# Kernel tuning notes

Hardware: AMD Instinct MI355X
Metric: run time of the kernel (lower is better)

The kernel has to match this reference:

```python
import jax, jax.numpy as jnp
import numpy as np

N = 50000; FIN = 64; H = 128; E = 800000; T = 8
P = 250000; D = 500000; G = 20000; V = 2000; O = 2


def _mp(h, Ws, Wn, b, edge_src, edge_dst, n):
    # mean-aggregation message passing: relu(h Ws + mean_neigh(h) Wn + b)
    deg = jax.ops.segment_sum(jnp.ones(edge_dst.shape[0], h.dtype), edge_dst, n)
    agg = jax.ops.segment_sum(h[edge_src], edge_dst, n) / jnp.maximum(deg, 1.0)[:, None]
    return jax.nn.relu(h @ Ws + agg @ Wn + b)


def _forward(x, W_enc_self, W_enc_nei, b_enc, W2_self, W2_nei, b2, Wd1, bd1, Wd2, bd2,
             counts, edge_src, edge_dst, place_idx, src_idx, t_idx, dst_nodes, dst_seg,
             group_id, variant_of_group):
    n = x.shape[0]
    p = place_idx.shape[0]
    g = variant_of_group.shape[0]
    v = counts.shape[0]
    # first encoder, then T sequential second_encoder applications (feature generations)
    h0 = _mp(x, W_enc_self, W_enc_nei, b_enc, edge_src, edge_dst, n)

    def step(h, _):
        h2 = _mp(h, W2_self, W2_nei, b2, edge_src, edge_dst, n)
        return h2, h2

    _, hs = jax.lax.scan(step, h0, None, length=T)
    feats = jnp.concatenate([h0[None], hs], axis=0)  # [T+1, N, H]

    # gather (place, src) features at the generation index of each prediction
    place_f = feats[t_idx, place_idx]                 # [P, H]
    src_f = feats[t_idx, src_idx]                     # [P, H]
    # dst feature = sum over the destination set of each prediction
    dst_f = jax.ops.segment_sum(feats[t_idx[dst_seg], dst_nodes], dst_seg, p)  # [P, H]

    cat = jnp.concatenate([place_f, src_f, dst_f], axis=-1)  # [P, 3H]
    logits = jax.nn.relu(cat @ Wd1 + bd1) @ Wd2 + bd2        # [P, O]
    logprob = jax.nn.log_softmax(logits, axis=-1)            # [P, O]

    # prev_prob: inclusive running sum of per-step logprob sums within each variant
    group_sums = jax.ops.segment_sum(logprob, group_id, g)   # [G, O]
    cum = jnp.cumsum(group_sums, axis=0)
    var_tot = jax.ops.segment_sum(group_sums, variant_of_group, v)
    var_excl = jnp.cumsum(var_tot, axis=0) - var_tot
    within = cum - var_excl[variant_of_group]                # [G, O]
    prev = within[group_id]                                  # [P, O]

    logc = jnp.log(counts / jnp.sum(counts))                 # log(count/total) per variant
    add = logprob + prev + logc[variant_of_group[group_id]][:, None]
    return jnp.zeros((n, logits.shape[-1]), x.dtype).at[place_idx].add(add)


def setup_inputs() -> dict:
    ks = jax.random.split(jax.random.key(0), 24)
    s = jnp.float32(0.05)
    f32 = jnp.float32
    i32 = jnp.int32
    return {
        "x": jax.random.normal(ks[0], (N, FIN), f32),
        "W_enc_self": jax.random.normal(ks[1], (FIN, H), f32) * s,
        "W_enc_nei": jax.random.normal(ks[2], (FIN, H), f32) * s,
        "b_enc": jax.random.normal(ks[3], (H,), f32) * s,
        "W2_self": jax.random.normal(ks[4], (H, H), f32) * s,
        "W2_nei": jax.random.normal(ks[5], (H, H), f32) * s,
        "b2": jax.random.normal(ks[6], (H,), f32) * s,
        "Wd1": jax.random.normal(ks[7], (3 * H, 3 * H), f32) * s,
        "bd1": jax.random.normal(ks[8], (3 * H,), f32) * s,
        "Wd2": jax.random.normal(ks[9], (3 * H, O), f32) * s,
        "bd2": jax.random.normal(ks[10], (O,), f32) * s,
        "counts": jax.random.uniform(ks[11], (V,), f32) + 0.5,
        "edge_src": jax.random.randint(ks[12], (E,), 0, N, i32),
        "edge_dst": jax.random.randint(ks[13], (E,), 0, N, i32),
        "place_idx": jax.random.randint(ks[14], (P,), 0, N, i32),
        "src_idx": jax.random.randint(ks[15], (P,), 0, N, i32),
        "t_idx": jax.random.randint(ks[16], (P,), 0, T + 1, i32),
        "dst_nodes": jax.random.randint(ks[17], (D,), 0, N, i32),
        "dst_seg": jnp.sort(jax.random.randint(ks[18], (D,), 0, P, i32)),
        "group_id": jnp.sort(jax.random.randint(ks[19], (P,), 0, G, i32)),
        "variant_of_group": jnp.sort(jax.random.randint(ks[20], (G,), 0, V, i32)),
    }


def reference(x, W_enc_self, W_enc_nei, b_enc, W2_self, W2_nei, b2, Wd1, bd1, Wd2, bd2,
              counts, edge_src, edge_dst, place_idx, src_idx, t_idx, dst_nodes, dst_seg,
              group_id, variant_of_group):
    return _forward(x, W_enc_self, W_enc_nei, b_enc, W2_self, W2_nei, b2, Wd1, bd1, Wd2, bd2,
                    counts, edge_src, edge_dst, place_idx, src_idx, t_idx, dst_nodes, dst_seg,
                    group_id, variant_of_group)
```

## Files before the change

### kernel.cpp

```cpp
#include <hip/hip_runtime.h>
#include <math.h>

#define NN 50000
#define FINN 64
#define HD 128
#define EE 800000
#define TT 8
#define PP 250000
#define DD 500000
#define GG 20000
#define VV 2000
#define OO 2

#define DEC_GRID 256
#define DEC_TILES ((PP + 63) / 64)

typedef short short8 __attribute__((ext_vector_type(8)));
typedef float f32x4 __attribute__((ext_vector_type(4)));

__device__ __forceinline__ unsigned short f2bf(float f) {
    unsigned int u = __float_as_uint(f);
    u += 0x7fffu + ((u >> 16) & 1u);
    return (unsigned short)(u >> 16);
}
__device__ __forceinline__ float bf2f(unsigned short u) {
    return __uint_as_float(((unsigned int)u) << 16);
}

struct us8 { unsigned short v[8]; };

__device__ __forceinline__ void gload_lds16(const void* g, void* l) {
    __builtin_amdgcn_global_load_lds((__attribute__((address_space(1))) void*)g,
                                     (__attribute__((address_space(3))) void*)l, 16, 0, 0);
}

__global__ void count_k(const int* __restrict__ idx, int* __restrict__ counts, int n) {
    int i = blockIdx.x * blockDim.x + threadIdx.x;
    if (i < n) atomicAdd(&counts[idx[i]], 1);
}

__global__ void blk_sum_k(const int* __restrict__ counts, int n, int* __restrict__ bsum) {
    __shared__ int buf[256];
    int t = threadIdx.x, i = blockIdx.x * 256 + t;
    buf[t] = (i < n) ? counts[i] : 0;
    __syncthreads();
    for (int off = 128; off > 0; off >>= 1) {
        if (t < off) buf[t] += buf[t + off];
        __syncthreads();
    }
    if (t == 0) bsum[blockIdx.x] = buf[0];
}

__global__ void scan_small_k(const int* __restrict__ bsum, int nb, int* __restrict__ boff) {
    __shared__ int buf[256];
    int t = threadIdx.x;
    int v = (t < nb) ? bsum[t] : 0;
    buf[t] = v;
    __syncthreads();
    for (int off = 1; off < 256; off <<= 1) {
        int u = (t >= off) ? buf[t - off] : 0;
        __syncthreads();
        buf[t] += u;
        __syncthreads();
    }
    if (t < nb) boff[t] = buf[t] - v;
}

__global__ void rowptr_fill_k(const int* __restrict__ counts, const int* __restrict__ boff,
                              int n, int* __restrict__ rowptr, int total) {
    __shared__ int buf[256];
    int t = threadIdx.x, i = blockIdx.x * 256 + t;
    int v = (i < n) ? counts[i] : 0;
    buf[t] = v;
    __syncthreads();
    for (int off = 1; off < 256; off <<= 1) {
        int u = (t >= off) ? buf[t - off] : 0;
        __syncthreads();
        buf[t] += u;
        __syncthreads();
    }
    if (i < n) rowptr[i] = boff[blockIdx.x] + buf[t] - v;
    if (i == 0) rowptr[n] = total;
}

__global__ void lb_rowptr_k(const int* __restrict__ arr, int n, int* __restrict__ rowptr, int m) {
    int i = blockIdx.x * blockDim.x + threadIdx.x;
    if (i > m) return;
    int lo = 0, hi = n;
    while (lo < hi) {
        int mid = (lo + hi) >> 1;
        if (arr[mid] < i) lo = mid + 1; else hi = mid;
    }
    rowptr[i] = lo;
}

__global__ void fill_csr_k(const int* __restrict__ esrc, const int* __restrict__ edst,
                           const int* __restrict__ rowptr, int* __restrict__ cursor,
                           int* __restrict__ outi, int n) {
    int e = blockIdx.x * blockDim.x + threadIdx.x;
    if (e < n) {
        int d = edst[e];
        int pos = atomicAdd(&cursor[d], 1);
        outi[rowptr[d] + pos] = esrc[e];
    }
}

__global__ void hist9_k(const int* __restrict__ t_idx, int* __restrict__ hist) {
    __shared__ int l[9];
    if (threadIdx.x < 9) l[threadIdx.x] = 0;
    __syncthreads();
    int p = blockIdx.x * 256 + threadIdx.x;
    if (p < PP) atomicAdd(&l[t_idx[p]], 1);
    __syncthreads();
    if (threadIdx.x < 9) atomicAdd(&hist[threadIdx.x], l[threadIdx.x]);
}

__global__ void scan9_k(const int* __restrict__ hist, int* __restrict__ boff9) {
    if (threadIdx.x == 0) {
        int a = 0;
        for (int i = 0; i < 9; ++i) { boff9[i] = a; a += hist[i]; }
    }
}

__global__ void bucket_perm_k(const int* __restrict__ t_idx, const int* __restrict__ boff9,
                              int* __restrict__ cursor9, int* __restrict__ pperm) {
    __shared__ int lcnt[9];
    __shared__ int lbase[9];
    int tid = threadIdx.x;
    int p = blockIdx.x * 256 + tid;
    if (tid < 9) lcnt[tid] = 0;
    __syncthreads();
    int t = 0, lr = 0;
    bool ok = p < PP;
    if (ok) {
        t = t_idx[p];
        lr = atomicAdd(&lcnt[t], 1);
    }
    __syncthreads();
    if (tid < 9) lbase[tid] = atomicAdd(&cursor9[tid], lcnt[tid]);
    __syncthreads();
    if (ok) pperm[boff9[t] + lbase[t] + lr] = p;
}

__global__ void prep_k(const float* __restrict__ x,
                       const float* __restrict__ Wes, const float* __restrict__ Wen,
                       const float* __restrict__ W2s, const float* __restrict__ W2n,
                       const float* __restrict__ Wd1,
                       unsigned short* __restrict__ xb, unsigned short* __restrict__ wenc_t,
                       unsigned short* __restrict__ w2_t, unsigned short* __restrict__ wd1t) {
    int i = blockIdx.x * 256 + threadIdx.x;
    if (i < NN * FINN) xb[i] = f2bf(x[i]);
    if (i < HD * 2 * FINN) {
        int c = i / (2 * FINN), k = i - c * (2 * FINN);
        wenc_t[i] = f2bf((k < FINN) ? Wes[k * HD + c] : Wen[(k - FINN) * HD + c]);
    }
    if (i < HD * 2 * HD) {
        int c = i / (2 * HD), k = i - c * (2 * HD);
        w2_t[i] = f2bf((k < HD) ? W2s[k * HD + c] : W2n[(k - HD) * HD + c]);
    }
    if (i < 384 * 384) {
        int n = i / 384, k = i - n * 384;
        wd1t[i] = f2bf(Wd1[k * 384 + n]);
    }
}

template <int KIN>
__launch_bounds__(256)
__global__ void agg2_k(const unsigned short* __restrict__ h, const int* __restrict__ rowptr,
                       const int* __restrict__ csr_src, unsigned short* __restrict__ aggout) {
    constexpr int LPR = KIN >> 3;
    constexpr int EPW = 64 / LPR;
    int node = blockIdx.x * 4 + (threadIdx.x >> 6);
    int lane = threadIdx.x & 63;
    int sub = lane / LPR;
    int fl = lane % LPR;
    if (node >= NN) return;
    int s = rowptr[node], e = rowptr[node + 1];
    float acc[8] = {};
    int i = s + sub;
    int iB = i + EPW;
    int srcA = (i < e) ? csr_src[i] : 0;
    int srcB = (iB < e) ? csr_src[iB] : 0;
    while (i < e) {
        bool hB = iB < e;
        us8 vA = *(const us8*)&h[(size_t)srcA * KIN + fl * 8];
        us8 vB;
        if (hB) vB = *(const us8*)&h[(size_t)srcB * KIN + fl * 8];
        int iN = iB + EPW, iN2 = iN + EPW;
        srcA = (iN < e) ? csr_src[iN] : 0;
        srcB = (iN2 < e) ? csr_src[iN2] : 0;
#pragma unroll
        for (int j = 0; j < 8; ++j) acc[j] += bf2f(vA.v[j]);
        if (hB) {
#pragma unroll
            for (int j = 0; j < 8; ++j) acc[j] += bf2f(vB.v[j]);
        }
        i = iN; iB = iN2;
    }
#pragma unroll
    for (int m = LPR; m < 64; m <<= 1)
#pragma unroll
        for (int j = 0; j < 8; ++j) acc[j] += __shfl_xor(acc[j], m);
    if (sub == 0) {
        float d = fmaxf((float)(e - s), 1.f);
        us8 o;
#pragma unroll
        for (int j = 0; j < 8; ++j) o.v[j] = f2bf(acc[j] / d);
        *(us8*)&aggout[(size_t)node * KIN + fl * 8] = o;
    }
}

__launch_bounds__(128)
__global__ void mp_mfma_k(const unsigned short* __restrict__ hin,
                          const unsigned short* __restrict__ aggin,
                          const unsigned short* __restrict__ Wt,
                          const float* __restrict__ bias,
                          unsigned short* __restrict__ hout, int Kin) {
    int tid = threadIdx.x;
    int lane = tid & 63, w = tid >> 6;
    int cc = lane & 15, g = lane >> 4;
    int K = 2 * Kin;
    int rowA = blockIdx.x * 32 + w * 16 + cc;
    bool rowok = rowA < NN;
    const unsigned short* hrow = hin + (size_t)rowA * Kin;
    const unsigned short* arow = aggin + (size_t)rowA * Kin;

    f32x4 acc[8];
#pragma unroll
    for (int t = 0; t < 8; ++t) acc[t] = (f32x4){0.f, 0.f, 0.f, 0.f};

    for (int k0 = 0; k0 < K; k0 += 32) {
        int k = k0 + g * 8;
        short8 a = {0, 0, 0, 0, 0, 0, 0, 0};
        if (rowok)
            a = *(const short8*)((k < Kin) ? (hrow + k) : (arow + (k - Kin)));
#pragma unroll
        for (int t = 0; t < 8; ++t) {
            short8 b = *(const short8*)&Wt[(size_t)(t * 16 + cc) * K + k];
            acc[t] = __builtin_amdgcn_mfma_f32_16x16x32_bf16(a, b, acc[t], 0, 0, 0);
        }
    }
#pragma unroll
    for (int t = 0; t < 8; ++t) {
        int col = t * 16 + cc;
        float b1 = bias[col];
#pragma unroll
        for (int r = 0; r < 4; ++r) {
            int grow = blockIdx.x * 32 + w * 16 + g * 4 + r;
            if (grow < NN)
                hout[(size_t)grow * HD + col] = f2bf(fmaxf(acc[t][r] + b1, 0.f));
        }
    }
}

__launch_bounds__(256)
__global__ void dst_sum2_k(const unsigned short* __restrict__ feats,
                           const int* __restrict__ t_idx, const int* __restrict__ dst_nodes,
                           const int* __restrict__ dst_rowptr, const int* __restrict__ pperm,
                           unsigned short* __restrict__ dstc) {
    int tid = threadIdx.x;
    int grp = tid >> 4;
    int fl = tid & 15;
    int pi = blockIdx.x * 16 + grp;
    if (pi >= PP) return;
    int p = pperm[pi];
    long t = t_idx[p];
    const unsigned short* base = feats + t * (long)NN * HD;
    int s = dst_rowptr[p], e = dst_rowptr[p + 1];
    float acc[8] = {};
    int i = s;
    int n0 = (i < e) ? dst_nodes[i] : 0;
    int n1 = (i + 1 < e) ? dst_nodes[i + 1] : 0;
    while (i < e) {
        bool h1 = (i + 1) < e;
        us8 v0 = *(const us8*)&base[(size_t)n0 * HD + fl * 8];
        us8 v1;
        if (h1) v1 = *(const us8*)&base[(size_t)n1 * HD + fl * 8];
        int i2 = i + 2, i3 = i + 3;
        n0 = (i2 < e) ? dst_nodes[i2] : 0;
        n1 = (i3 < e) ? dst_nodes[i3] : 0;
#pragma unroll
        for (int j = 0; j < 8; ++j) acc[j] += bf2f(v0.v[j]);
        if (h1) {
#pragma unroll
            for (int j = 0; j < 8; ++j) acc[j] += bf2f(v1.v[j]);
        }
        i = i2;
    }
    us8 o;
#pragma unroll
    for (int j = 0; j < 8; ++j) o.v[j] = f2bf(acc[j]);
    *(us8*)&dstc[(size_t)pi * HD + fl * 8] = o;
}

__launch_bounds__(256, 1)
__global__ void dec5_k(const unsigned short* __restrict__ feats,
                       const unsigned short* __restrict__ dstc,
                       const int* __restrict__ place_idx, const int* __restrict__ src_idx,
                       const int* __restrict__ t_idx, const int* __restrict__ group_id,
                       const int* __restrict__ pperm,
                       const unsigned short* __restrict__ Wd1t,
                       const float* __restrict__ bd1, const float* __restrict__ Wd2,
                       const float* __restrict__ bd2, float* __restrict__ logprob,
                       float* __restrict__ group_sums) {
    __shared__ unsigned short buf[3][192 * 128];
    __shared__ unsigned long long rb[3][192];
    __shared__ float lpart[2][4][64][2];

    int tid = threadIdx.x;
    int lane = tid & 63, w = tid >> 6;
    int cc = lane & 15, gq = lane >> 4;
    int cx7 = cc & 7;
    int bid = blockIdx.x;

    int row = min(tid, 191);
    int sec = row >> 6, pl = row & 63;
    const int* nptr = (sec == 0) ? place_idx : src_idx;

    int nt = (DEC_TILES - 1 - bid) / DEC_GRID + 1;

    float b20 = bd2[0], b21 = bd2[1];

    int pic0 = min((bid + 0 * DEC_GRID) * 64 + pl, PP - 1);
    int pic1 = min((bid + 1 * DEC_GRID) * 64 + pl, PP - 1);
    int pic2 = min((bid + 2 * DEC_GRID) * 64 + pl, PP - 1);
    int pA = pperm[pic0], pB = pperm[pic1], pC = pperm[pic2];
    int preg = pperm[min((bid + 3 * DEC_GRID) * 64 + pl, PP - 1)];
    if (tid < 192) {
        rb[0][tid] = (sec == 2) ? (unsigned long long)(dstc + (size_t)pic0 * HD)
                                : (unsigned long long)(feats + (((long)t_idx[pA] * NN + nptr[pA]) * (long)HD));
        rb[1][tid] = (sec == 2) ? (unsigned long long)(dstc + (size_t)pic1 * HD)
                                : (unsigned long long)(feats + (((long)t_idx[pB] * NN + nptr[pB]) * (long)HD));
        rb[2][tid] = (sec == 2) ? (unsigned long long)(dstc + (size_t)pic2 * HD)
                                : (unsigned long long)(feats + (((long)t_idx[pC] * NN + nptr[pC]) * (long)HD));
    }

    short8 breg[72];
    {
        const unsigned short* bbase = Wd1t + ((long)(w * 96 + cc) * 384 + gq * 8);
#pragma unroll
        for (int kk = 0; kk < 12; ++kk)
#pragma unroll
            for (int t = 0; t < 6; ++t)
                breg[kk * 6 + t] = *(const short8*)(bbase + (long)t * 16 * 384 + kk * 32);
    }
    __syncthreads();

    int rsub = lane >> 4, chunk = lane & 15;

#define STAGE(slot_)                                                                 \
    {                                                                                \
        _Pragma("unroll")                                                            \
        for (int i = 0; i < 12; ++i) {                                               \
            int r = w * 48 + i * 4 + rsub;                                           \
            const unsigned short* src =                                              \
                (const unsigned short*)rb[slot_][r] + ((chunk ^ (r & 7)) * 8);       \
            gload_lds16(src, &buf[slot_][(w * 48 + i * 4) * 128]);                   \
        }                                                                            \
    }

#define OUTPUT(tlo_, po_)                                                            \
    if (lane < 16) {                                                                 \
        int orow = w * 16 + cc;                                                      \
        int pi = (tlo_) * 64 + orow;                                                 \
        if (pi < PP) {                                                               \
            int p = pperm[pi];                                                       \
            float l0 = lpart[po_][0][orow][0] + lpart[po_][1][orow][0] +             \
                       lpart[po_][2][orow][0] + lpart[po_][3][orow][0] + b20;        \
            float l1 = lpart[po_][0][orow][1] + lpart[po_][1][orow][1] +             \
                       lpart[po_][2][orow][1] + lpart[po_][3][orow][1] + b21;        \
            float mm = fmaxf(l0, l1);                                                \
            float lse = mm + logf(expf(l0 - mm) + expf(l1 - mm));                    \
            float lp0 = l0 - lse, lp1 = l1 - lse;                                    \
            logprob[p * 2 + 0] = lp0;                                                \
            logprob[p * 2 + 1] = lp1;                                                \
            int g = group_id[p];                                                     \
            atomicAdd(&group_sums[g * 2 + 0], lp0);                                  \
            atomicAdd(&group_sums[g * 2 + 1], lp1);                                  \
        }                                                                            \
    }

    STAGE(0);
    STAGE(1);

    for (int k = 0; k < nt; ++k) {
        int par = k % 3;

        int tload = t_idx[preg];
        int nload = nptr[preg];
        int preg2 = pperm[min((bid + (k + 4) * DEC_GRID) * 64 + pl, PP - 1)];
        int picw = min((bid + (k + 3) * DEC_GRID) * 64 + pl, PP - 1);

        if (k + 2 < nt) STAGE((k + 2) % 3);

        __builtin_amdgcn_sched_barrier(0);
        if (k + 2 < nt) {
            asm volatile("s_waitcnt vmcnt(27)" ::: "memory");
        } else if (k + 1 < nt) {
            asm volatile("s_waitcnt vmcnt(18)" ::: "memory");
        } else {
            asm volatile("s_waitcnt vmcnt(6)" ::: "memory");
        }
        __builtin_amdgcn_s_barrier();
        __builtin_amdgcn_sched_barrier(0);

        if (k > 0) {
            int tprev = bid + (k - 1) * DEC_GRID;
            OUTPUT(tprev, (k - 1) & 1);
        }

        const unsigned short* bufc = &buf[par][0];
        f32x4 acc[4][6];
#pragma unroll
        for (int s = 0; s < 4; ++s)
#pragma unroll
            for (int t = 0; t < 6; ++t) acc[s][t] = (f32x4){0.f, 0.f, 0.f, 0.f};

#pragma unroll
        for (int kk = 0; kk < 12; ++kk) {
            int seck = kk >> 2;
            int cbase = (kk & 3) * 4 + gq;
            int coff = (cbase ^ cx7) * 8;
            short8 a_c[4];
#pragma unroll
            for (int s = 0; s < 4; ++s) {
                int lrow = seck * 64 + s * 16 + cc;
                a_c[s] = *(const short8*)&bufc[lrow * 128 + coff];
            }
#pragma unroll
            for (int t = 0; t < 6; ++t)
#pragma unroll
                for (int s = 0; s < 4; ++s)
                    acc[s][t] = __builtin_amdgcn_mfma_f32_16x16x32_bf16(a_c[s], breg[kk * 6 + t],
                                                                        acc[s][t], 0, 0, 0);
        }

        float part[4][4][2] = {};
#pragma unroll
        for (int t = 0; t < 6; ++t) {
            int col = w * 96 + t * 16 + cc;
            float b1 = bd1[col];
            float w0 = Wd2[col * 2 + 0], w1 = Wd2[col * 2 + 1];
#pragma unroll
            for (int s = 0; s < 4; ++s)
#pragma unroll
                for (int r = 0; r < 4; ++r) {
                    float h = fmaxf(acc[s][t][r] + b1, 0.f);
                    part[s][r][0] += h * w0;
                    part[s][r][1] += h * w1;
                }
        }
#pragma unroll
        for (int m = 1; m < 16; m <<= 1)
#pragma unroll
            for (int s = 0; s < 4; ++s)
#pragma unroll
                for (int r = 0; r < 4; ++r) {
                    part[s][r][0] += __shfl_xor(part[s][r][0], m);
                    part[s][r][1] += __shfl_xor(part[s][r][1], m);
                }
        if (cc == 0) {
#pragma unroll
            for (int s = 0; s < 4; ++s)
#pragma unroll
                for (int r = 0; r < 4; ++r) {
                    int orow = s * 16 + gq * 4 + r;
                    lpart[k & 1][w][orow][0] = part[s][r][0];
                    lpart[k & 1][w][orow][1] = part[s][r][1];
                }
        }

        if (tid < 192)
            rb[par][tid] = (sec == 2)
                               ? (unsigned long long)(dstc + (size_t)picw * HD)
                               : (unsigned long long)(feats + (((long)tload * NN + nload) * (long)HD));
        preg = preg2;

        asm volatile("s_waitcnt lgkmcnt(0)" ::: "memory");
        __builtin_amdgcn_s_barrier();
        __builtin_amdgcn_sched_barrier(0);
    }

    {
        int tlast = bid + (nt - 1) * DEC_GRID;
        OUTPUT(tlast, (nt - 1) & 1);
    }
#undef STAGE
#undef OUTPUT
}

__global__ void within_total_k(const float* __restrict__ group_sums,
                               const int* __restrict__ var_rowptr,
                               const float* __restrict__ counts,
                               float* __restrict__ within, float* __restrict__ total) {
    __shared__ float buf[256];
    int tid = threadIdx.x;
    float s = 0.f;
    for (int i = tid; i < VV; i += 256) s += counts[i];
    buf[tid] = s;
    __syncthreads();
    for (int off = 128; off > 0; off >>= 1) {
        if (tid < off) buf[tid] += buf[tid + off];
        __syncthreads();
    }
    if (tid == 0) total[0] = buf[0];
    for (int v = tid; v < VV; v += 256) {
        int gs = var_rowptr[v], ge = var_rowptr[v + 1];
        float r0 = 0.f, r1 = 0.f;
        for (int g = gs; g < ge; ++g) {
            r0 += group_sums[2 * g + 0];
            r1 += group_sums[2 * g + 1];
            within[2 * g + 0] = r0;
            within[2 * g + 1] = r1;
        }
    }
}

__global__ void final_k(const float* __restrict__ logprob, const float* __restrict__ within,
                        const int* __restrict__ group_id, const int* __restrict__ vog,
                        const float* __restrict__ counts, const float* __restrict__ total,
                        const int* __restrict__ place_idx, float* __restrict__ outp) {
    int p = blockIdx.x * blockDim.x + threadIdx.x;
    if (p >= PP) return;
    int g = group_id[p];
    int v = vog[g];
    float lc = logf(counts[v]) - logf(total[0]);
    int node = place_idx[p];
    atomicAdd(&outp[node * 2 + 0], logprob[p * 2 + 0] + within[g * 2 + 0] + lc);
    atomicAdd(&outp[node * 2 + 1], logprob[p * 2 + 1] + within[g * 2 + 1] + lc);
}

extern "C" void kernel_launch(void* const* d_in, const int* in_sizes, int n_in,
                              void* d_out, int out_size, void* d_ws, size_t ws_size,
                              hipStream_t stream) {
    const float* x          = (const float*)d_in[0];
    const float* W_enc_self = (const float*)d_in[1];
    const float* W_enc_nei  = (const float*)d_in[2];
    const float* b_enc      = (const float*)d_in[3];
    const float* W2_self    = (const float*)d_in[4];
    const float* W2_nei     = (const float*)d_in[5];
    const float* b2         = (const float*)d_in[6];
    const float* Wd1        = (const float*)d_in[7];
    const float* bd1        = (const float*)d_in[8];
    const float* Wd2        = (const float*)d_in[9];
    const float* bd2        = (const float*)d_in[10];
    const float* counts     = (const float*)d_in[11];
    const int* edge_src     = (const int*)d_in[12];
    const int* edge_dst     = (const int*)d_in[13];
    const int* place_idx    = (const int*)d_in[14];
    const int* src_idx      = (const int*)d_in[15];
    const int* t_idx        = (const int*)d_in[16];
    const int* dst_nodes    = (const int*)d_in[17];
    const int* dst_seg      = (const int*)d_in[18];
    const int* group_id     = (const int*)d_in[19];
    const int* variant_of_group = (const int*)d_in[20];
    float* outp = (float*)d_out;

    const int NB = (NN + 255) / 256;

    unsigned short* feats = (unsigned short*)d_ws;
    unsigned short* aggb  = feats + (size_t)(TT + 1) * NN * HD;
    unsigned short* xb    = aggb + (size_t)NN * HD;
    unsigned short* dstc  = xb + (size_t)NN * FINN;
    unsigned short* wenc_t = dstc + (size_t)PP * HD;
    unsigned short* w2_t   = wenc_t + HD * 2 * FINN;
    unsigned short* wd1t   = w2_t + HD * 2 * HD;
    int* zr = (int*)(wd1t + 384 * 384);
    int* csr_counts   = zr;
    int* csr_cursor   = csr_counts + NN;
    float* group_sums = (float*)(csr_cursor + NN);
    int* hist9        = (int*)(group_sums + 2 * GG);
    int* cursor9      = hist9 + 9;
    size_t zero_words = (size_t)NN + NN + 2 * GG + 18;
    int* bsum       = cursor9 + 9;
    int* boff       = bsum + 256;
    int* boff9      = boff + 256;
    int* csr_rowptr = boff9 + 16;
    int* dst_rowptr = csr_rowptr + (NN + 1);
    int* var_rowptr = dst_rowptr + (PP + 1);
    int* csr_src    = var_rowptr + (VV + 1);
    int* pperm      = csr_src + EE;
    float* logprob  = (float*)(pperm + PP);
    float* within   = logprob + 2 * PP;
    float* total_counts = within + 2 * GG;

    hipMemsetAsync(zr, 0, zero_words * 4, stream);
    hipMemsetAsync(d_out, 0, (size_t)out_size * sizeof(float), stream);

    prep_k<<<(NN * FINN + 255) / 256, 256, 0, stream>>>(x, W_enc_self, W_enc_nei, W2_self,
                                                        W2_nei, Wd1, xb, wenc_t, w2_t, wd1t);
    count_k<<<(EE + 255) / 256, 256, 0, stream>>>(edge_dst, csr_counts, EE);
    blk_sum_k<<<NB, 256, 0, stream>>>(csr_counts, NN, bsum);
    scan_small_k<<<1, 256, 0, stream>>>(bsum, NB, boff);
    rowptr_fill_k<<<NB, 256, 0, stream>>>(csr_counts, boff, NN, csr_rowptr, EE);
    fill_csr_k<<<(EE + 255) / 256, 256, 0, stream>>>(edge_src, edge_dst, csr_rowptr,
                                                     csr_cursor, csr_src, EE);
    lb_rowptr_k<<<(PP + 256) / 256, 256, 0, stream>>>(dst_seg, DD, dst_rowptr, PP);
    lb_rowptr_k<<<(VV + 256) / 256, 256, 0, stream>>>(variant_of_group, GG, var_rowptr, VV);
    hist9_k<<<(PP + 255) / 256, 256, 0, stream>>>(t_idx, hist9);
    scan9_k<<<1, 64, 0, stream>>>(hist9, boff9);
    bucket_perm_k<<<(PP + 255) / 256, 256, 0, stream>>>(t_idx, boff9, cursor9, pperm);

    for (int r = 0; r <= TT; ++r) {
        const unsigned short* hin = (r == 0) ? xb : feats + (size_t)(r - 1) * NN * HD;
        unsigned short* hout = feats + (size_t)r * NN * HD;
        if (r == 0) {
            agg2_k<FINN><<<(NN + 3) / 4, 256, 0, stream>>>(hin, csr_rowptr, csr_src, aggb);
            mp_mfma_k<<<(NN + 31) / 32, 128, 0, stream>>>(hin, aggb, wenc_t, b_enc, hout, FINN);
        } else {
            agg2_k<HD><<<(NN + 3) / 4, 256, 0, stream>>>(hin, csr_rowptr, csr_src, aggb);
            mp_mfma_k<<<(NN + 31) / 32, 128, 0, stream>>>(hin, aggb, w2_t, b2, hout, HD);
        }
    }

    dst_sum2_k<<<(PP + 15) / 16, 256, 0, stream>>>(feats, t_idx, dst_nodes, dst_rowptr, pperm, dstc);
    dec5_k<<<DEC_GRID, 256, 0, stream>>>(feats, dstc, place_idx, src_idx, t_idx,
                                         group_id, pperm, wd1t, bd1, Wd2, bd2,
                                         logprob, group_sums);

    within_total_k<<<1, 256, 0, stream>>>(group_sums, var_rowptr, counts, within, total_counts);
    final_k<<<(PP + 255) / 256, 256, 0, stream>>>(logprob, within, group_id, variant_of_group,
                                                  counts, total_counts, place_idx, outp);
}
```

Measured before the change: 1.049 ms.

## Fuse neighbor aggregation into MFMA layer kernel and widen decoder to 512 threads

Merges the separate mean-aggregation and message-passing GEMM kernels into one kernel. Each block gathers neighbor means for its 32 nodes into swizzled LDS and feeds them straight to the MFMA, so the aggregated bf16 buffer no longer makes a round trip through global memory. The decoder now runs 8 waves per block, each holding half as many weight registers. It stores 32-bit row offsets instead of 64-bit pointers, prefetches permutation, group and index lookups further ahead, and keeps three slots of partial logits. The risks are fewer lanes per node during the gather and the 32-bit offset assumption about the relative placement of the feature and dst buffers.

```diff
diff --git a/kernel.cpp b/kernel.cpp
--- a/kernel.cpp
+++ b/kernel.cpp
@@ -166,89 +166,104 @@
 
 template <int KIN>
 __launch_bounds__(256)
-__global__ void agg2_k(const unsigned short* __restrict__ h, const int* __restrict__ rowptr,
-                       const int* __restrict__ csr_src, unsigned short* __restrict__ aggout) {
-    constexpr int LPR = KIN >> 3;
-    constexpr int EPW = 64 / LPR;
-    int node = blockIdx.x * 4 + (threadIdx.x >> 6);
-    int lane = threadIdx.x & 63;
-    int sub = lane / LPR;
-    int fl = lane % LPR;
-    if (node >= NN) return;
-    int s = rowptr[node], e = rowptr[node + 1];
-    float acc[8] = {};
-    int i = s + sub;
-    int iB = i + EPW;
-    int srcA = (i < e) ? csr_src[i] : 0;
-    int srcB = (iB < e) ? csr_src[iB] : 0;
-    while (i < e) {
-        bool hB = iB < e;
-        us8 vA = *(const us8*)&h[(size_t)srcA * KIN + fl * 8];
-        us8 vB;
-        if (hB) vB = *(const us8*)&h[(size_t)srcB * KIN + fl * 8];
-        int iN = iB + EPW, iN2 = iN + EPW;
-        srcA = (iN < e) ? csr_src[iN] : 0;
-        srcB = (iN2 < e) ? csr_src[iN2] : 0;
-#pragma unroll
-        for (int j = 0; j < 8; ++j) acc[j] += bf2f(vA.v[j]);
-        if (hB) {
-#pragma unroll
-            for (int j = 0; j < 8; ++j) acc[j] += bf2f(vB.v[j]);
-        }
-        i = iN; iB = iN2;
-    }
-#pragma unroll
-    for (int m = LPR; m < 64; m <<= 1)
-#pragma unroll
-        for (int j = 0; j < 8; ++j) acc[j] += __shfl_xor(acc[j], m);
-    if (sub == 0) {
+__global__ void mpf_k(const unsigned short* __restrict__ hin,
+                      const int* __restrict__ rowptr, const int* __restrict__ csr_src,
+                      const unsigned short* __restrict__ Wt, const float* __restrict__ bias,
+                      unsigned short* __restrict__ hout) {
+    constexpr int CPL = KIN / 64;
+    __shared__ unsigned short sm[32 * KIN];
+    int tid = threadIdx.x;
+    int r = tid >> 3;
+    int sl = tid & 7;
+    int node = blockIdx.x * 32 + r;
+    int rx = r & 7;
+
+    if (node < NN) {
+        int s = rowptr[node], e = rowptr[node + 1];
+        float acc[8 * CPL] = {};
+        int i = s, iB = s + 1;
+        int srcA = (i < e) ? csr_src[i] : 0;
+        int srcB = (iB < e) ? csr_src[iB] : 0;
+        while (i < e) {
+            bool hB = iB < e;
+            us8 vA0, vA1, vB0, vB1;
+            vA0 = *(const us8*)&hin[(size_t)srcA * KIN + sl * (8 * CPL)];
+            if constexpr (CPL == 2) vA1 = *(const us8*)&hin[(size_t)srcA * KIN + sl * 16 + 8];
+            if (hB) {
+                vB0 = *(const us8*)&hin[(size_t)srcB * KIN + sl * (8 * CPL)];
+                if constexpr (CPL == 2) vB1 = *(const us8*)&hin[(size_t)srcB * KIN + sl * 16 + 8];
+            }
+            int iN = i + 2, iN2 = i + 3;
+            srcA = (iN < e) ? csr_src[iN] : 0;
+            srcB = (iN2 < e) ? csr_src[iN2] : 0;
+#pragma unroll
+            for (int j = 0; j < 8; ++j) acc[j] += bf2f(vA0.v[j]);
+            if constexpr (CPL == 2)
+#pragma unroll
+                for (int j = 0; j < 8; ++j) acc[8 + j] += bf2f(vA1.v[j]);
+            if (hB) {
+#pragma unroll
+                for (int j = 0; j < 8; ++j) acc[j] += bf2f(vB0.v[j]);
+                if constexpr (CPL == 2)
+#pragma unroll
+                    for (int j = 0; j < 8; ++j) acc[8 + j] += bf2f(vB1.v[j]);
+            }
+            i = iN; iB = iN2;
+        }
         float d = fmaxf((float)(e - s), 1.f);
-        us8 o;
-#pragma unroll
-        for (int j = 0; j < 8; ++j) o.v[j] = f2bf(acc[j] / d);
-        *(us8*)&aggout[(size_t)node * KIN + fl * 8] = o;
-    }
-}
-
-__launch_bounds__(128)
-__global__ void mp_mfma_k(const unsigned short* __restrict__ hin,
-                          const unsigned short* __restrict__ aggin,
-                          const unsigned short* __restrict__ Wt,
-                          const float* __restrict__ bias,
-                          unsigned short* __restrict__ hout, int Kin) {
-    int tid = threadIdx.x;
+        us8 o0, o1;
+#pragma unroll
+        for (int j = 0; j < 8; ++j) o0.v[j] = f2bf(acc[j] / d);
+        int c0 = sl * CPL;
+        *(us8*)&sm[r * KIN + ((c0 ^ rx) * 8)] = o0;
+        if constexpr (CPL == 2) {
+#pragma unroll
+            for (int j = 0; j < 8; ++j) o1.v[j] = f2bf(acc[8 + j] / d);
+            *(us8*)&sm[r * KIN + (((c0 + 1) ^ rx) * 8)] = o1;
+        }
+    }
+    __syncthreads();
+
     int lane = tid & 63, w = tid >> 6;
-    int cc = lane & 15, g = lane >> 4;
-    int K = 2 * Kin;
-    int rowA = blockIdx.x * 32 + w * 16 + cc;
+    int cc = lane & 15, gq = lane >> 4;
+    constexpr int K = 2 * KIN;
+    int rloc = (w & 1) * 16 + cc;
+    int rowA = blockIdx.x * 32 + rloc;
     bool rowok = rowA < NN;
-    const unsigned short* hrow = hin + (size_t)rowA * Kin;
-    const unsigned short* arow = aggin + (size_t)rowA * Kin;
-
-    f32x4 acc[8];
-#pragma unroll
-    for (int t = 0; t < 8; ++t) acc[t] = (f32x4){0.f, 0.f, 0.f, 0.f};
-
+    const unsigned short* hrow = hin + (size_t)rowA * KIN;
+    int ch = (w >> 1) * 64;
+    int rlx = rloc & 7;
+
+    f32x4 acc2[4];
+#pragma unroll
+    for (int t = 0; t < 4; ++t) acc2[t] = (f32x4){0.f, 0.f, 0.f, 0.f};
+
+#pragma unroll
     for (int k0 = 0; k0 < K; k0 += 32) {
-        int k = k0 + g * 8;
+        int k = k0 + gq * 8;
         short8 a = {0, 0, 0, 0, 0, 0, 0, 0};
-        if (rowok)
-            a = *(const short8*)((k < Kin) ? (hrow + k) : (arow + (k - Kin)));
-#pragma unroll
-        for (int t = 0; t < 8; ++t) {
-            short8 b = *(const short8*)&Wt[(size_t)(t * 16 + cc) * K + k];
-            acc[t] = __builtin_amdgcn_mfma_f32_16x16x32_bf16(a, b, acc[t], 0, 0, 0);
-        }
-    }
-#pragma unroll
-    for (int t = 0; t < 8; ++t) {
-        int col = t * 16 + cc;
+        if (rowok) {
+            if (k0 < KIN) a = *(const short8*)(hrow + k);
+            else {
+                int chunk = (k - KIN) >> 3;
+                a = *(const short8*)&sm[rloc * KIN + ((chunk ^ rlx) * 8)];
+            }
+        }
+#pragma unroll
+        for (int t = 0; t < 4; ++t) {
+            short8 b = *(const short8*)&Wt[(size_t)(ch + t * 16 + cc) * K + k];
+            acc2[t] = __builtin_amdgcn_mfma_f32_16x16x32_bf16(a, b, acc2[t], 0, 0, 0);
+        }
+    }
+#pragma unroll
+    for (int t = 0; t < 4; ++t) {
+        int col = ch + t * 16 + cc;
         float b1 = bias[col];
 #pragma unroll
-        for (int r = 0; r < 4; ++r) {
-            int grow = blockIdx.x * 32 + w * 16 + g * 4 + r;
+        for (int rj = 0; rj < 4; ++rj) {
+            int grow = blockIdx.x * 32 + (w & 1) * 16 + gq * 4 + rj;
             if (grow < NN)
-                hout[(size_t)grow * HD + col] = f2bf(fmaxf(acc[t][r] + b1, 0.f));
+                hout[(size_t)grow * HD + col] = f2bf(fmaxf(acc2[t][rj] + b1, 0.f));
         }
     }
 }
@@ -293,8 +308,8 @@
     *(us8*)&dstc[(size_t)pi * HD + fl * 8] = o;
 }
 
-__launch_bounds__(256, 1)
-__global__ void dec5_k(const unsigned short* __restrict__ feats,
+__launch_bounds__(512, 2)
+__global__ void dec6_k(const unsigned short* __restrict__ feats,
                        const unsigned short* __restrict__ dstc,
                        const int* __restrict__ place_idx, const int* __restrict__ src_idx,
                        const int* __restrict__ t_idx, const int* __restrict__ group_id,
@@ -304,45 +319,52 @@
                        const float* __restrict__ bd2, float* __restrict__ logprob,
                        float* __restrict__ group_sums) {
     __shared__ unsigned short buf[3][192 * 128];
-    __shared__ unsigned long long rb[3][192];
-    __shared__ float lpart[2][4][64][2];
+    __shared__ unsigned int rb[3][192];
+    __shared__ float lpart[3][8][64][2];
 
     int tid = threadIdx.x;
     int lane = tid & 63, w = tid >> 6;
     int cc = lane & 15, gq = lane >> 4;
-    int cx7 = cc & 7;
     int bid = blockIdx.x;
 
     int row = min(tid, 191);
     int sec = row >> 6, pl = row & 63;
     const int* nptr = (sec == 0) ? place_idx : src_idx;
+    unsigned int dstc_off = (unsigned int)((const char*)dstc - (const char*)feats);
 
     int nt = (DEC_TILES - 1 - bid) / DEC_GRID + 1;
-
     float b20 = bd2[0], b21 = bd2[1];
 
-    int pic0 = min((bid + 0 * DEC_GRID) * 64 + pl, PP - 1);
-    int pic1 = min((bid + 1 * DEC_GRID) * 64 + pl, PP - 1);
-    int pic2 = min((bid + 2 * DEC_GRID) * 64 + pl, PP - 1);
-    int pA = pperm[pic0], pB = pperm[pic1], pC = pperm[pic2];
-    int preg = pperm[min((bid + 3 * DEC_GRID) * 64 + pl, PP - 1)];
     if (tid < 192) {
-        rb[0][tid] = (sec == 2) ? (unsigned long long)(dstc + (size_t)pic0 * HD)
-                                : (unsigned long long)(feats + (((long)t_idx[pA] * NN + nptr[pA]) * (long)HD));
-        rb[1][tid] = (sec == 2) ? (unsigned long long)(dstc + (size_t)pic1 * HD)
-                                : (unsigned long long)(feats + (((long)t_idx[pB] * NN + nptr[pB]) * (long)HD));
-        rb[2][tid] = (sec == 2) ? (unsigned long long)(dstc + (size_t)pic2 * HD)
-                                : (unsigned long long)(feats + (((long)t_idx[pC] * NN + nptr[pC]) * (long)HD));
-    }
-
-    short8 breg[72];
+#pragma unroll
+        for (int s3 = 0; s3 < 3; ++s3) {
+            int pic = min((bid + s3 * DEC_GRID) * 64 + pl, PP - 1);
+            int p = pperm[pic];
+            rb[s3][tid] = (sec == 2) ? (dstc_off + (unsigned int)pic * 256u)
+                                     : (unsigned int)(((unsigned)t_idx[p] * NN + (unsigned)nptr[p]) * 256u);
+        }
+    }
+    int p3 = pperm[min((bid + 3 * DEC_GRID) * 64 + pl, PP - 1)];
+    int tOld = t_idx[p3], nOld = nptr[p3];
+    int pCur = pperm[min((bid + 4 * DEC_GRID) * 64 + pl, PP - 1)];
+    int opPP = 0, opP = 0, ogP = 0;
+
+    short8 breg[36];
+    float b1r[3], w0r[3], w1r[3];
     {
-        const unsigned short* bbase = Wd1t + ((long)(w * 96 + cc) * 384 + gq * 8);
+        const unsigned short* bbase = Wd1t + ((long)(w * 48 + cc) * 384 + gq * 8);
 #pragma unroll
         for (int kk = 0; kk < 12; ++kk)
 #pragma unroll
-            for (int t = 0; t < 6; ++t)
-                breg[kk * 6 + t] = *(const short8*)(bbase + (long)t * 16 * 384 + kk * 32);
+            for (int t = 0; t < 3; ++t)
+                breg[kk * 3 + t] = *(const short8*)(bbase + (long)t * 16 * 384 + kk * 32);
+#pragma unroll
+        for (int t = 0; t < 3; ++t) {
+            int col = w * 48 + t * 16 + cc;
+            b1r[t] = bd1[col];
+            w0r[t] = Wd2[col * 2 + 0];
+            w1r[t] = Wd2[col * 2 + 1];
+        }
     }
     __syncthreads();
 
@@ -351,32 +373,31 @@
 #define STAGE(slot_)                                                                 \
     {                                                                                \
         _Pragma("unroll")                                                            \
-        for (int i = 0; i < 12; ++i) {                                               \
-            int r = w * 48 + i * 4 + rsub;                                           \
-            const unsigned short* src =                                              \
-                (const unsigned short*)rb[slot_][r] + ((chunk ^ (r & 7)) * 8);       \
-            gload_lds16(src, &buf[slot_][(w * 48 + i * 4) * 128]);                   \
+        for (int i = 0; i < 6; ++i) {                                                \
+            int r = w * 24 + i * 4 + rsub;                                           \
+            const char* src = (const char*)feats + rb[slot_][r] +                    \
+                              ((unsigned)(chunk ^ (r & 7)) << 4);                    \
+            gload_lds16(src, &buf[slot_][(w * 24 + i * 4) * 128]);                   \
         }                                                                            \
     }
 
-#define OUTPUT(tlo_, po_)                                                            \
-    if (lane < 16) {                                                                 \
-        int orow = w * 16 + cc;                                                      \
-        int pi = (tlo_) * 64 + orow;                                                 \
+#define OUTPUT(tile_, slot_, opv_, ogv_)                                             \
+    {                                                                                \
+        int pi = (bid + (tile_) * DEC_GRID) * 64 + w * 16 + cc;                      \
         if (pi < PP) {                                                               \
-            int p = pperm[pi];                                                       \
-            float l0 = lpart[po_][0][orow][0] + lpart[po_][1][orow][0] +             \
-                       lpart[po_][2][orow][0] + lpart[po_][3][orow][0] + b20;        \
-            float l1 = lpart[po_][0][orow][1] + lpart[po_][1][orow][1] +             \
-                       lpart[po_][2][orow][1] + lpart[po_][3][orow][1] + b21;        \
+            float l0 = b20, l1 = b21;                                                \
+            _Pragma("unroll")                                                        \
+            for (int w2 = 0; w2 < 8; ++w2) {                                         \
+                l0 += lpart[slot_][w2][w * 16 + cc][0];                              \
+                l1 += lpart[slot_][w2][w * 16 + cc][1];                              \
+            }                                                                        \
             float mm = fmaxf(l0, l1);                                                \
             float lse = mm + logf(expf(l0 - mm) + expf(l1 - mm));                    \
             float lp0 = l0 - lse, lp1 = l1 - lse;                                    \
-            logprob[p * 2 + 0] = lp0;                                                \
-            logprob[p * 2 + 1] = lp1;                                                \
-            int g = group_id[p];                                                     \
-            atomicAdd(&group_sums[g * 2 + 0], lp0);                                  \
-            atomicAdd(&group_sums[g * 2 + 1], lp1);                                  \
+            logprob[(opv_)*2 + 0] = lp0;                                             \
+            logprob[(opv_)*2 + 1] = lp1;                                             \
+            atomicAdd(&group_sums[(ogv_)*2 + 0], lp0);                               \
+            atomicAdd(&group_sums[(ogv_)*2 + 1], lp1);                               \
         }                                                                            \
     }
 
@@ -384,106 +405,109 @@
     STAGE(1);
 
     for (int k = 0; k < nt; ++k) {
-        int par = k % 3;
-
-        int tload = t_idx[preg];
-        int nload = nptr[preg];
-        int preg2 = pperm[min((bid + (k + 4) * DEC_GRID) * 64 + pl, PP - 1)];
-        int picw = min((bid + (k + 3) * DEC_GRID) * 64 + pl, PP - 1);
+        int slot = k % 3;
+
+        int opN = pperm[min((bid + k * DEC_GRID) * 64 + (w & 3) * 16 + cc, PP - 1)];
+        int ogN = group_id[opP];
+        int pNew = pperm[min((bid + (k + 5) * DEC_GRID) * 64 + pl, PP - 1)];
+        int tNew = t_idx[pCur];
+        int nNew = nptr[pCur];
+        __builtin_amdgcn_sched_barrier(0);
 
         if (k + 2 < nt) STAGE((k + 2) % 3);
-
         __builtin_amdgcn_sched_barrier(0);
+
         if (k + 2 < nt) {
-            asm volatile("s_waitcnt vmcnt(27)" ::: "memory");
+            if (k >= 2) { asm volatile("s_waitcnt vmcnt(21)" ::: "memory"); }
+            else        { asm volatile("s_waitcnt vmcnt(17)" ::: "memory"); }
         } else if (k + 1 < nt) {
-            asm volatile("s_waitcnt vmcnt(18)" ::: "memory");
+            asm volatile("s_waitcnt vmcnt(15)" ::: "memory");
         } else {
-            asm volatile("s_waitcnt vmcnt(6)" ::: "memory");
+            asm volatile("s_waitcnt vmcnt(5)" ::: "memory");
         }
         __builtin_amdgcn_s_barrier();
         __builtin_amdgcn_sched_barrier(0);
 
-        if (k > 0) {
-            int tprev = bid + (k - 1) * DEC_GRID;
-            OUTPUT(tprev, (k - 1) & 1);
-        }
-
-        const unsigned short* bufc = &buf[par][0];
-        f32x4 acc[4][6];
-#pragma unroll
-        for (int s = 0; s < 4; ++s)
-#pragma unroll
-            for (int t = 0; t < 6; ++t) acc[s][t] = (f32x4){0.f, 0.f, 0.f, 0.f};
-
-#pragma unroll
-        for (int kk = 0; kk < 12; ++kk) {
-            int seck = kk >> 2;
-            int cbase = (kk & 3) * 4 + gq;
-            int coff = (cbase ^ cx7) * 8;
-            short8 a_c[4];
-#pragma unroll
-            for (int s = 0; s < 4; ++s) {
-                int lrow = seck * 64 + s * 16 + cc;
-                a_c[s] = *(const short8*)&bufc[lrow * 128 + coff];
+        if (k >= 2 && w < 4 && lane < 16) OUTPUT(k - 2, (k - 2) % 3, opPP, ogP);
+
+        {
+            const unsigned short* bufc = &buf[slot][0];
+            f32x4 acc[4][3];
+#pragma unroll
+            for (int s = 0; s < 4; ++s)
+#pragma unroll
+                for (int t = 0; t < 3; ++t) acc[s][t] = (f32x4){0.f, 0.f, 0.f, 0.f};
+
+#pragma unroll
+            for (int kk = 0; kk < 12; ++kk) {
+                int seck = kk >> 2;
+                int cbase = (kk & 3) * 4 + gq;
+                int coff = (cbase ^ (cc & 7)) * 8;
+                short8 a_c[4];
+#pragma unroll
+                for (int s = 0; s < 4; ++s) {
+                    int lrow = seck * 64 + s * 16 + cc;
+                    a_c[s] = *(const short8*)&bufc[lrow * 128 + coff];
+                }
+#pragma unroll
+                for (int t = 0; t < 3; ++t)
+#pragma unroll
+                    for (int s = 0; s < 4; ++s)
+                        acc[s][t] = __builtin_amdgcn_mfma_f32_16x16x32_bf16(
+                            a_c[s], breg[kk * 3 + t], acc[s][t], 0, 0, 0);
             }
-#pragma unroll
-            for (int t = 0; t < 6; ++t)
+
+            float part[4][4][2] = {};
+#pragma unroll
+            for (int t = 0; t < 3; ++t) {
 #pragma unroll
                 for (int s = 0; s < 4; ++s)
-                    acc[s][t] = __builtin_amdgcn_mfma_f32_16x16x32_bf16(a_c[s], breg[kk * 6 + t],
-                                                                        acc[s][t], 0, 0, 0);
-        }
-
-        float part[4][4][2] = {};
-#pragma unroll
-        for (int t = 0; t < 6; ++t) {
-            int col = w * 96 + t * 16 + cc;
-            float b1 = bd1[col];
-            float w0 = Wd2[col * 2 + 0], w1 = Wd2[col * 2 + 1];
-#pragma unroll
-            for (int s = 0; s < 4; ++s)
-#pragma unroll
-                for (int r = 0; r < 4; ++r) {
-                    float h = fmaxf(acc[s][t][r] + b1, 0.f);
-                    part[s][r][0] += h * w0;
-                    part[s][r][1] += h * w1;
-                }
-        }
-#pragma unroll
-        for (int m = 1; m < 16; m <<= 1)
-#pragma unroll
-            for (int s = 0; s < 4; ++s)
-#pragma unroll
-                for (int r = 0; r < 4; ++r) {
-                    part[s][r][0] += __shfl_xor(part[s][r][0], m);
-                    part[s][r][1] += __shfl_xor(part[s][r][1], m);
-                }
-        if (cc == 0) {
-#pragma unroll
-            for (int s = 0; s < 4; ++s)
-#pragma unroll
-                for (int r = 0; r < 4; ++r) {
-                    int orow = s * 16 + gq * 4 + r;
-                    lpart[k & 1][w][orow][0] = part[s][r][0];
-                    lpart[k & 1][w][orow][1] = part[s][r][1];
-                }
-        }
-
-        if (tid < 192)
-            rb[par][tid] = (sec == 2)
-                               ? (unsigned long long)(dstc + (size_t)picw * HD)
-                               : (unsigned long long)(feats + (((long)tload * NN + nload) * (long)HD));
-        preg = preg2;
+#pragma unroll
+                    for (int r = 0; r < 4; ++r) {
+                        float h = fmaxf(acc[s][t][r] + b1r[t], 0.f);
+                        part[s][r][0] += h * w0r[t];
+                        part[s][r][1] += h * w1r[t];
+                    }
+            }
+#pragma unroll
+            for (int m = 1; m < 16; m <<= 1)
+#pragma unroll
+                for (int s = 0; s < 4; ++s)
+#pragma unroll
+                    for (int r = 0; r < 4; ++r) {
+                        part[s][r][0] += __shfl_xor(part[s][r][0], m);
+                        part[s][r][1] += __shfl_xor(part[s][r][1], m);
+                    }
+            if (cc == 0) {
+#pragma unroll
+                for (int s = 0; s < 4; ++s)
+#pragma unroll
+                    for (int r = 0; r < 4; ++r) {
+                        int orow = s * 16 + gq * 4 + r;
+                        lpart[slot][w][orow][0] = part[s][r][0];
+                        lpart[slot][w][orow][1] = part[s][r][1];
+                    }
+            }
+        }
+
+        if (tid < 192) {
+            int picw = min((bid + (k + 3) * DEC_GRID) * 64 + pl, PP - 1);
+            rb[(k + 3) % 3][tid] = (sec == 2)
+                ? (dstc_off + (unsigned int)picw * 256u)
+                : (unsigned int)(((unsigned)tOld * NN + (unsigned)nOld) * 256u);
+        }
+        tOld = tNew; nOld = nNew; pCur = pNew;
+        opPP = opP; opP = opN; ogP = ogN;
 
         asm volatile("s_waitcnt lgkmcnt(0)" ::: "memory");
         __builtin_amdgcn_s_barrier();
         __builtin_amdgcn_sched_barrier(0);
     }
 
-    {
-        int tlast = bid + (nt - 1) * DEC_GRID;
-        OUTPUT(tlast, (nt - 1) & 1);
+    if (w < 4 && lane < 16) {
+        OUTPUT(nt - 2, (nt - 2) % 3, opPP, ogP);
+        int ogLast = group_id[opP];
+        OUTPUT(nt - 1, (nt - 1) % 3, opP, ogLast);
     }
 #undef STAGE
 #undef OUTPUT
@@ -601,20 +625,18 @@
     scan9_k<<<1, 64, 0, stream>>>(hist9, boff9);
     bucket_perm_k<<<(PP + 255) / 256, 256, 0, stream>>>(t_idx, boff9, cursor9, pperm);
 
+    const int NB32 = (NN + 31) / 32;
     for (int r = 0; r <= TT; ++r) {
         const unsigned short* hin = (r == 0) ? xb : feats + (size_t)(r - 1) * NN * HD;
         unsigned short* hout = feats + (size_t)r * NN * HD;
-        if (r == 0) {
-            agg2_k<FINN><<<(NN + 3) / 4, 256, 0, stream>>>(hin, csr_rowptr, csr_src, aggb);
-            mp_mfma_k<<<(NN + 31) / 32, 128, 0, stream>>>(hin, aggb, wenc_t, b_enc, hout, FINN);
-        } else {
-            agg2_k<HD><<<(NN + 3) / 4, 256, 0, stream>>>(hin, csr_rowptr, csr_src, aggb);
-            mp_mfma_k<<<(NN + 31) / 32, 128, 0, stream>>>(hin, aggb, w2_t, b2, hout, HD);
-        }
+        if (r == 0)
+            mpf_k<FINN><<<NB32, 256, 0, stream>>>(hin, csr_rowptr, csr_src, wenc_t, b_enc, hout);
+        else
+            mpf_k<HD><<<NB32, 256, 0, stream>>>(hin, csr_rowptr, csr_src, w2_t, b2, hout);
     }
 
     dst_sum2_k<<<(PP + 15) / 16, 256, 0, stream>>>(feats, t_idx, dst_nodes, dst_rowptr, pperm, dstc);
-    dec5_k<<<DEC_GRID, 256, 0, stream>>>(feats, dstc, place_idx, src_idx, t_idx,
+    dec6_k<<<DEC_GRID, 512, 0, stream>>>(feats, dstc, place_idx, src_idx, t_idx,
                                          group_id, pperm, wd1t, bd1, Wd2, bd2,
                                          logprob, group_sums);
 
```

Result: faster. 989.7 us (-5.6%).
